# Optimization experiments

Measured on AMD Instinct MI355X. Metric: run time of the kernel, lower is better.

Reference implementation:

```python
import jax, jax.numpy as jnp
import numpy as np

N_USER = 100000
N_ITEM = 100000
N_TAG = 10000
DIM = 128
E_BUYS = 1_000_000
E_REV = 1_000_000
E_TAGS = 1_000_000
W_SCALE = 0.05


def setup_inputs() -> dict:
    key = jax.random.key(0)
    ks = jax.random.split(key, 18)
    inp = {
        "x_user": jax.random.normal(ks[0], (N_USER, DIM), jnp.float32),
        "x_item": jax.random.normal(ks[1], (N_ITEM, DIM), jnp.float32),
        "x_tag": jax.random.normal(ks[2], (N_TAG, DIM), jnp.float32),
        # edge_index per relation: row 0 = src node ids, row 1 = dst node ids
        "ei_buys": jnp.stack([
            jax.random.randint(ks[3], (E_BUYS,), 0, N_USER, jnp.int32),
            jax.random.randint(ks[4], (E_BUYS,), 0, N_ITEM, jnp.int32)]),
        "ei_rev": jnp.stack([
            jax.random.randint(ks[5], (E_REV,), 0, N_ITEM, jnp.int32),
            jax.random.randint(ks[6], (E_REV,), 0, N_USER, jnp.int32)]),
        "ei_tags": jnp.stack([
            jax.random.randint(ks[7], (E_TAGS,), 0, N_TAG, jnp.int32),
            jax.random.randint(ks[8], (E_TAGS,), 0, N_ITEM, jnp.int32)]),
    }
    # SAGEConv params per edge type: lin_l (neighbor agg), lin_r (root), bias
    names = ["buys", "rev", "tags"]
    for i, n in enumerate(names):
        inp[f"Wl_{n}"] = jax.random.normal(ks[9 + 3 * i], (DIM, DIM), jnp.float32) * W_SCALE
        inp[f"Wr_{n}"] = jax.random.normal(ks[10 + 3 * i], (DIM, DIM), jnp.float32) * W_SCALE
        inp[f"b_{n}"] = jnp.zeros((DIM,), jnp.float32)
    return inp


def _sage(x_src, x_dst, ei, Wl, Wr, b):
    """SAGEConv with mean neighbor aggregation: lin_l(mean_j x_j) + lin_r(x_i) + b."""
    n_dst = x_dst.shape[0]
    src, dst = ei[0], ei[1]
    msg_sum = jax.ops.segment_sum(x_src[src], dst, num_segments=n_dst)  # [n_dst, D]
    cnt = jax.ops.segment_sum(jnp.ones(src.shape, x_src.dtype), dst, num_segments=n_dst)
    msg_mean = msg_sum / jnp.maximum(cnt, 1.0)[:, None]
    return msg_mean @ Wl + x_dst @ Wr + b


def reference(x_user, x_item, x_tag, ei_buys, ei_rev, ei_tags,
              Wl_buys, Wr_buys, b_buys,
              Wl_rev, Wr_rev, b_rev,
              Wl_tags, Wr_tags, b_tags):
    # per-relation SAGEConv
    o_item_buys = _sage(x_user, x_item, ei_buys, Wl_buys, Wr_buys, b_buys)
    o_user = _sage(x_item, x_user, ei_rev, Wl_rev, Wr_rev, b_rev)
    o_item_tags = _sage(x_tag, x_item, ei_tags, Wl_tags, Wr_tags, b_tags)
    # HeteroConv aggr='mean' across edge types per destination node type
    out_item = 0.5 * (o_item_buys + o_item_tags)
    out_user = o_user  # single relation into 'user'
    return (out_user, out_item)
```

## Files before the change

### kernel.cpp

```cpp
#include <hip/hip_runtime.h>
#include <hip/hip_bf16.h>
#include <stdint.h>

#define DIM 128
#define NNODE 100000
#define NB 98
#define NBT (3 * NB)
#define T_TILE 8192

typedef __attribute__((ext_vector_type(8))) short short8;
typedef __attribute__((ext_vector_type(4))) float f32x4;

__device__ __forceinline__ unsigned short f32_to_bf16_rne(float f) {
    union { float f; uint32_t u; } v; v.f = f;
    uint32_t u = v.u;
    uint32_t r = u + 0x7FFFu + ((u >> 16) & 1u);
    return (unsigned short)(r >> 16);
}

__global__ void conv_kernel(const float* __restrict__ xu, const float* __restrict__ xi,
                            const float* __restrict__ xt,
                            unsigned short* __restrict__ bu, unsigned short* __restrict__ bi,
                            unsigned short* __restrict__ bt, int nu, int ni, int nt) {
    int idx = blockIdx.x * blockDim.x + threadIdx.x;
    int q_u = nu >> 2, q_i = ni >> 2, q_t = nt >> 2;
    const float* src; unsigned short* dst; int o;
    if (idx < q_u)                { src = xu; dst = bu; o = idx; }
    else if (idx < q_u + q_i)     { src = xi; dst = bi; o = idx - q_u; }
    else if (idx < q_u + q_i+q_t) { src = xt; dst = bt; o = idx - q_u - q_i; }
    else return;
    float4 f = ((const float4*)src)[o];
    ushort4 u;
    u.x = f32_to_bf16_rne(f.x); u.y = f32_to_bf16_rne(f.y);
    u.z = f32_to_bf16_rne(f.z); u.w = f32_to_bf16_rne(f.w);
    ((ushort4*)dst)[o] = u;
}

__global__ __launch_bounds__(256) void coarse_hist(
    const int* __restrict__ ei0, const int* __restrict__ ei1, const int* __restrict__ ei2,
    int E0, int E1, int E2, int* __restrict__ ccnt) {
    __shared__ int h[NBT];
    int Etot = E0 + E1 + E2;
    for (int i = threadIdx.x; i < NBT; i += 256) h[i] = 0;
    __syncthreads();
    for (int e = blockIdx.x * blockDim.x + threadIdx.x; e < Etot; e += gridDim.x * blockDim.x) {
        int rel, le; const int* ei; int E;
        if (e < E0)           { rel = 0; le = e;           ei = ei0; E = E0; }
        else if (e < E0 + E1) { rel = 1; le = e - E0;      ei = ei1; E = E1; }
        else                  { rel = 2; le = e - E0 - E1; ei = ei2; E = E2; }
        int d = ei[E + le];
        atomicAdd(&h[rel * NB + (d >> 10)], 1);
    }
    __syncthreads();
    for (int i = threadIdx.x; i < NBT; i += 256) {
        int c = h[i];
        if (c) atomicAdd(&ccnt[i], c);
    }
}

__global__ __launch_bounds__(512) void coarse_scan(const int* __restrict__ ccnt,
                                                   int* __restrict__ bases,
                                                   int* __restrict__ cursor) {
    __shared__ int s[512];
    int t = threadIdx.x;
    int v = (t < NBT) ? ccnt[t] : 0;
    s[t] = v;
    __syncthreads();
    for (int d = 1; d < 512; d <<= 1) {
        int x = (t >= d) ? s[t - d] : 0;
        __syncthreads();
        s[t] += x;
        __syncthreads();
    }
    int excl = s[t] - v;
    if (t < NBT) { bases[t] = excl; cursor[t] = excl; }
    if (t == NBT) bases[NBT] = excl;
}

__global__ __launch_bounds__(256) void coarse_scatter(
    const int* __restrict__ ei0, const int* __restrict__ ei1, const int* __restrict__ ei2,
    int E0, int E1, int E2, int* __restrict__ cursor, int* __restrict__ pairs) {
    __shared__ int h[NBT], hb[NBT], lc[NBT];
    int Etot = E0 + E1 + E2;
    int ntiles = (Etot + T_TILE - 1) / T_TILE;
    for (int tile = blockIdx.x; tile < ntiles; tile += gridDim.x) {
        int tbase = tile * T_TILE;
        for (int i = threadIdx.x; i < NBT; i += 256) { h[i] = 0; lc[i] = 0; }
        __syncthreads();
        int binreg[32], valreg[32];
        #pragma unroll
        for (int k = 0; k < 32; k++) {
            int e = tbase + k * 256 + threadIdx.x;
            binreg[k] = -1;
            if (e < Etot) {
                int rel, le; const int* ei; int E;
                if (e < E0)           { rel = 0; le = e;           ei = ei0; E = E0; }
                else if (e < E0 + E1) { rel = 1; le = e - E0;      ei = ei1; E = E1; }
                else                  { rel = 2; le = e - E0 - E1; ei = ei2; E = E2; }
                int d = ei[E + le];
                int s = ei[le];
                int bin = rel * NB + (d >> 10);
                binreg[k] = bin;
                valreg[k] = s | ((d & 1023) << 17);
                atomicAdd(&h[bin], 1);
            }
        }
        __syncthreads();
        for (int i = threadIdx.x; i < NBT; i += 256) {
            int c = h[i];
            hb[i] = c ? atomicAdd(&cursor[i], c) : 0;
        }
        __syncthreads();
        #pragma unroll
        for (int k = 0; k < 32; k++) {
            if (binreg[k] >= 0) {
                int bin = binreg[k];
                int pos = hb[bin] + atomicAdd(&lc[bin], 1);
                pairs[pos] = valreg[k];
            }
        }
        __syncthreads();
    }
}

__global__ __launch_bounds__(256) void fine_sort(
    const int* __restrict__ bases, const int* __restrict__ pairs,
    int* __restrict__ off, int* __restrict__ sorted, int N) {
    __shared__ int h[1024], ho[1024], ssum[256];
    int b = blockIdx.x;
    int rel = b / NB, jb = b - rel * NB;
    int ebase = bases[b], ne = bases[b + 1] - ebase;
    int dbase = jb << 10;
    int tid = threadIdx.x;
    for (int i = tid; i < 1024; i += 256) h[i] = 0;
    __syncthreads();
    for (int i = tid; i < ne; i += 256) {
        int dl = pairs[ebase + i] >> 17;
        atomicAdd(&h[dl], 1);
    }
    __syncthreads();
    int v0 = h[tid * 4], v1 = h[tid * 4 + 1], v2 = h[tid * 4 + 2], v3 = h[tid * 4 + 3];
    int tsum = v0 + v1 + v2 + v3;
    ssum[tid] = tsum;
    __syncthreads();
    for (int s = 1; s < 256; s <<= 1) {
        int t = (tid >= s) ? ssum[tid - s] : 0;
        __syncthreads();
        ssum[tid] += t;
        __syncthreads();
    }
    int excl = ssum[tid] - tsum;
    ho[tid * 4] = excl;
    ho[tid * 4 + 1] = excl + v0;
    ho[tid * 4 + 2] = excl + v0 + v1;
    ho[tid * 4 + 3] = excl + v0 + v1 + v2;
    __syncthreads();
    for (int i = tid; i < 1024; i += 256) {
        int d = dbase + i;
        if (d < N) off[rel * N + d] = ebase + ho[i];
        h[i] = 0;
    }
    __syncthreads();
    for (int i = tid; i < ne; i += 256) {
        int p = pairs[ebase + i];
        int dl = p >> 17;
        int pos = ebase + ho[dl] + atomicAdd(&h[dl], 1);
        sorted[pos] = p & 0x1FFFF;
    }
}

__global__ __launch_bounds__(256) void agg_mfma(
    const unsigned short* __restrict__ xb_user, const unsigned short* __restrict__ xb_item,
    const unsigned short* __restrict__ xb_tag,
    const int* __restrict__ sorted, const int* __restrict__ off,
    unsigned short* __restrict__ msg, int N, int Etot) {
    __shared__ __align__(1024) unsigned char smem[4][9216];
    const int wid = threadIdx.x >> 6;
    const int lane = threadIdx.x & 63;
    const int grp = blockIdx.x * 4 + wid;
    const int ngrp = (3 * N) >> 4;
    if (grp >= ngrp) return;
    const int g0 = grp << 4;
    const int rel = (g0 >= 2 * N) ? 2 : ((g0 >= N) ? 1 : 0);
    const unsigned short* xs = (rel == 0) ? xb_user : (rel == 1) ? xb_item : xb_tag;

    unsigned char* stage = smem[wid];
    unsigned char* segb  = smem[wid] + 8192;
    int* bnd = (int*)(smem[wid] + 8192 + 768);

    if (lane < 17) {
        int idx = g0 + lane;
        bnd[lane] = (idx < 3 * N) ? off[idx] : Etot;
    }
    const int b0 = bnd[0];
    const int L  = bnd[16] - b0;
    int nchunk = (L + 31) >> 5;
    if (nchunk > 20) nchunk = 20;
    const int tot = nchunk << 5;

    for (int i = lane; i < tot; i += 64) {
        int k = b0 + i;
        int s = 0;
        #pragma unroll
        for (int t = 1; t <= 16; t++) s += (k >= bnd[t]) ? 1 : 0;
        segb[i] = (unsigned char)s;
    }

    const int jsel = (lane & 7) >> 1;
    const int laneoff = ((lane >> 3) << 5) + ((lane & 1) << 4);
    const unsigned int stage_u =
        (unsigned int)(size_t)(__attribute__((address_space(3))) unsigned char*)stage;
    const unsigned int tb = stage_u + ((lane >> 4) << 11) + ((lane & 15) << 3);
    const unsigned char* xsb = (const unsigned char*)xs;

    f32x4 acc[8];
    #pragma unroll
    for (int i = 0; i < 8; i++) acc[i] = (f32x4){0.f, 0.f, 0.f, 0.f};

    for (int c = 0; c < nchunk; c++) {
        const int cb = b0 + (c << 5);
        int kk = cb + (lane & 31);
        kk = (kk < Etot) ? kk : (Etot - 1);
        const int sv = sorted[kk];
        #pragma unroll
        for (int q = 0; q < 8; q++) {
            int srow = __shfl(sv, (q << 2) + jsel, 64);
            const unsigned char* gp = xsb + (((size_t)srow) << 8) + laneoff;
            __builtin_amdgcn_global_load_lds(
                (const __attribute__((address_space(1))) unsigned int*)gp,
                (__attribute__((address_space(3))) unsigned int*)(stage + (q << 10)),
                16, 0, 0);
        }
        const unsigned long long sg =
            *(const unsigned long long*)(segb + (c << 5) + ((lane >> 4) << 3));
        short8 af;
        #pragma unroll
        for (int j = 0; j < 8; j++)
            af[j] = ((int)((sg >> (j << 3)) & 0xFFull) == (lane & 15)) ? (short)0x3F80 : (short)0;

        asm volatile("s_waitcnt vmcnt(0)" ::: "memory");
        unsigned long long blo[8], bhi[8];
        #pragma unroll
        for (int nt = 0; nt < 8; nt++) {
            asm volatile("ds_read_b64_tr_b16 %0, %2\n\t"
                         "ds_read_b64_tr_b16 %1, %2 offset:1024"
                         : "=&v"(blo[nt]), "=&v"(bhi[nt]) : "v"(tb + (nt << 7)));
        }
        asm volatile("s_waitcnt lgkmcnt(0)" ::: "memory");
        __builtin_amdgcn_sched_barrier(0);
        #pragma unroll
        for (int nt = 0; nt < 8; nt++) {
            union { unsigned long long u[2]; short8 s; } cv;
            cv.u[0] = blo[nt]; cv.u[1] = bhi[nt];
            acc[nt] = __builtin_amdgcn_mfma_f32_16x16x32_bf16(af, cv.s, acc[nt], 0, 0, 0);
        }
    }

    const int gq = lane >> 4;
    const int fc = lane & 15;
    int dg[5];
    #pragma unroll
    for (int r = 0; r < 5; r++) dg[r] = bnd[(gq << 2) + r];
    float invd[4];
    #pragma unroll
    for (int r = 0; r < 4; r++) {
        int d = dg[r + 1] - dg[r];
        invd[r] = 1.0f / (float)(d > 0 ? d : 1);
    }
    unsigned short* outb = (unsigned short*)stage;
    #pragma unroll
    for (int nt = 0; nt < 8; nt++) {
        #pragma unroll
        for (int r = 0; r < 4; r++) {
            outb[(((gq << 2) + r) << 7) + (nt << 4) + fc] =
                f32_to_bf16_rne(acc[nt][r] * invd[r]);
        }
    }
    unsigned char* mp = (unsigned char*)(msg + ((size_t)g0 << 7));
    #pragma unroll
    for (int s = 0; s < 4; s++) {
        uint4 vv = *(const uint4*)(stage + (s << 10) + (lane << 4));
        *(uint4*)(mp + (s << 10) + (lane << 4)) = vv;
    }
}

__global__ void pack_kernel(const float* __restrict__ Wl_b, const float* __restrict__ Wr_b,
                            const float* __restrict__ b_b,
                            const float* __restrict__ Wl_r, const float* __restrict__ Wr_r,
                            const float* __restrict__ b_r,
                            const float* __restrict__ Wl_t, const float* __restrict__ Wr_t,
                            const float* __restrict__ b_t,
                            unsigned short* __restrict__ pw_item,
                            unsigned short* __restrict__ pw_user,
                            float* __restrict__ bias_item, float* __restrict__ bias_user) {
    const int NI = 12 * 8 * 64 * 8;
    const int NU = 8 * 8 * 64 * 8;
    int o = blockIdx.x * blockDim.x + threadIdx.x;
    if (o < NI) {
        int j = o & 7, lane = (o >> 3) & 63, ks = o >> 12;
        int n = ((o >> 9) & 7) * 16 + (lane & 15);
        int k = (ks & 3) * 32 + (lane >> 4) * 8 + j;
        int src = ks >> 2;
        float v;
        if (src == 0)      v = 0.5f * Wl_b[k * DIM + n];
        else if (src == 1) v = 0.5f * Wl_t[k * DIM + n];
        else               v = 0.5f * (Wr_b[k * DIM + n] + Wr_t[k * DIM + n]);
        pw_item[o] = f32_to_bf16_rne(v);
    } else if (o < NI + NU) {
        int oo = o - NI;
        int j = oo & 7, lane = (oo >> 3) & 63, ks = oo >> 12;
        int n = ((oo >> 9) & 7) * 16 + (lane & 15);
        int k = (ks & 3) * 32 + (lane >> 4) * 8 + j;
        float v = ((ks >> 2) == 0) ? Wl_r[k * DIM + n] : Wr_r[k * DIM + n];
        pw_user[oo] = f32_to_bf16_rne(v);
    } else {
        int oo = o - NI - NU;
        if (oo < DIM)            bias_item[oo] = 0.5f * (b_b[oo] + b_t[oo]);
        else if (oo < 2 * DIM)   bias_user[oo - DIM] = b_r[oo - DIM];
    }
}

__global__ __launch_bounds__(256) void gemm_kernel(
    const unsigned short* __restrict__ Abf0,
    const unsigned short* __restrict__ Abf1,
    const unsigned short* __restrict__ Abf2,
    int n_src,
    const unsigned short* __restrict__ packW,
    const float* __restrict__ bias,
    float* __restrict__ out, int M) {
    int wave = threadIdx.x >> 6;
    int lane = threadIdx.x & 63;
    int quad = lane >> 4;
    int l15  = lane & 15;
    int m0   = blockIdx.x * 64 + wave * 16;
    int arow = m0 + l15;
    bool arow_ok = arow < M;
    int nks = n_src * 4;

    f32x4 acc[8];
    #pragma unroll
    for (int i = 0; i < 8; i++) acc[i] = (f32x4){0.f, 0.f, 0.f, 0.f};

    for (int ks = 0; ks < nks; ks++) {
        int src = ks >> 2;
        int kofs = (ks & 3) * 32 + quad * 8;
        short8 afrag;
        const unsigned short* A = (src == 0) ? Abf0 : (src == 1) ? Abf1 : Abf2;
        if (arow_ok) afrag = *(const short8*)(A + (size_t)arow * DIM + kofs);
        else         afrag = (short8){0,0,0,0,0,0,0,0};
        const unsigned short* wp = packW + ((size_t)ks * 8 * 64 + lane) * 8;
        #pragma unroll
        for (int nt = 0; nt < 8; nt++) {
            short8 wfrag = *(const short8*)(wp + (size_t)nt * 64 * 8);
            acc[nt] = __builtin_amdgcn_mfma_f32_16x16x32_bf16(afrag, wfrag, acc[nt], 0, 0, 0);
        }
    }
    #pragma unroll
    for (int nt = 0; nt < 8; nt++) {
        int col = nt * 16 + l15;
        float bv = bias[col];
        #pragma unroll
        for (int r = 0; r < 4; r++) {
            int row = m0 + quad * 4 + r;
            if (row < M) out[(size_t)row * DIM + col] = acc[nt][r] + bv;
        }
    }
}

extern "C" void kernel_launch(void* const* d_in, const int* in_sizes, int n_in,
                              void* d_out, int out_size, void* d_ws, size_t ws_size,
                              hipStream_t stream) {
    const float* x_user = (const float*)d_in[0];
    const float* x_item = (const float*)d_in[1];
    const float* x_tag  = (const float*)d_in[2];
    const int* ei_buys  = (const int*)d_in[3];
    const int* ei_rev   = (const int*)d_in[4];
    const int* ei_tags  = (const int*)d_in[5];
    const float* Wl_b = (const float*)d_in[6];
    const float* Wr_b = (const float*)d_in[7];
    const float* b_b  = (const float*)d_in[8];
    const float* Wl_r = (const float*)d_in[9];
    const float* Wr_r = (const float*)d_in[10];
    const float* b_r  = (const float*)d_in[11];
    const float* Wl_t = (const float*)d_in[12];
    const float* Wr_t = (const float*)d_in[13];
    const float* b_t  = (const float*)d_in[14];

    const int N  = NNODE;
    const int E0 = in_sizes[3] / 2, E1 = in_sizes[4] / 2, E2 = in_sizes[5] / 2;
    const int n_user = in_sizes[0], n_item = in_sizes[1], n_tag = in_sizes[2];

    char* w = (char*)d_ws;
    int* off    = (int*)(w + 1200000);
    int* ccnt   = (int*)(w + 2400000);
    int* bases  = (int*)(w + 2401280);
    int* cursor = (int*)(w + 2402560);
    int* sorted = (int*)(w + 2403840);
    unsigned short* msg = (unsigned short*)(w + 15600000);
    int* pairs  = (int*)(w + 15600000);
    unsigned short* pw_item = (unsigned short*)(w + 92400000);
    unsigned short* pw_user = (unsigned short*)(w + 92498304);
    float* bias_item = (float*)(w + 92563840);
    float* bias_user = (float*)(w + 92564352);
    unsigned short* xb_user = (unsigned short*)(w + 92564992);
    unsigned short* xb_item = (unsigned short*)(w + 118164992);
    unsigned short* xb_tag  = (unsigned short*)(w + 143764992);

    float* out_user = (float*)d_out;
    float* out_item = out_user + (size_t)N * DIM;

    int Etot = E0 + E1 + E2;

    hipMemsetAsync(ccnt, 0, NBT * sizeof(int), stream);

    pack_kernel<<<(49152 + 32768 + 2 * DIM + 255) / 256, 256, 0, stream>>>(
        Wl_b, Wr_b, b_b, Wl_r, Wr_r, b_r, Wl_t, Wr_t, b_t,
        pw_item, pw_user, bias_item, bias_user);

    int tot4 = (n_user + n_item + n_tag) / 4;
    conv_kernel<<<(tot4 + 255) / 256, 256, 0, stream>>>(
        x_user, x_item, x_tag, xb_user, xb_item, xb_tag, n_user, n_item, n_tag);

    coarse_hist<<<512, 256, 0, stream>>>(ei_buys, ei_rev, ei_tags, E0, E1, E2, ccnt);

    coarse_scan<<<1, 512, 0, stream>>>(ccnt, bases, cursor);

    int ntiles = (Etot + T_TILE - 1) / T_TILE;
    coarse_scatter<<<ntiles, 256, 0, stream>>>(
        ei_buys, ei_rev, ei_tags, E0, E1, E2, cursor, pairs);

    fine_sort<<<NBT, 256, 0, stream>>>(bases, pairs, off, sorted, N);

    int ngrp = (3 * N) / 16;
    agg_mfma<<<(ngrp + 3) / 4, 256, 0, stream>>>(
        xb_user, xb_item, xb_tag, sorted, off, msg, N, Etot);

    gemm_kernel<<<(N + 63) / 64, 256, 0, stream>>>(
        msg, msg + 2 * (size_t)N * DIM, xb_item, 3, pw_item, bias_item, out_item, N);

    gemm_kernel<<<(N + 63) / 64, 256, 0, stream>>>(
        msg + (size_t)N * DIM, xb_user, nullptr, 2, pw_user, bias_user, out_user, N);
}
```

Measured before the change: 493.0 us.

## Double-buffer gather-to-LDS in MFMA aggregation with software-pipelined chunk pairs

Restructures the agg_mfma inner loop to process two 32-edge chunks per iteration. Each chunk gets its own 8 KB LDS staging buffer, and the global_load_lds gathers for the next chunk are issued right after the MFMAs on the current buffer, with partial vmcnt waits in place of a full drain. The sorted-index loads are prefetched one iteration ahead. To fit the doubled LDS per wave, the block shrinks from 4 to 3 waves, which changes occupancy. The goal is to hide gather latency behind MFMA work, at the cost of more LDS per wave and extra speculative loads when the chunk count is odd.

```diff
diff --git a/kernel.cpp b/kernel.cpp
--- a/kernel.cpp
+++ b/kernel.cpp
@@ -7,6 +7,8 @@
 #define NB 98
 #define NBT (3 * NB)
 #define T_TILE 8192
+#define AGG_NW 3
+#define AGG_WLDS 17408
 
 typedef __attribute__((ext_vector_type(8))) short short8;
 typedef __attribute__((ext_vector_type(4))) float f32x4;
@@ -169,15 +171,15 @@
     }
 }
 
-__global__ __launch_bounds__(256) void agg_mfma(
+__global__ __launch_bounds__(192) void agg_mfma(
     const unsigned short* __restrict__ xb_user, const unsigned short* __restrict__ xb_item,
     const unsigned short* __restrict__ xb_tag,
     const int* __restrict__ sorted, const int* __restrict__ off,
     unsigned short* __restrict__ msg, int N, int Etot) {
-    __shared__ __align__(1024) unsigned char smem[4][9216];
+    __shared__ __align__(1024) unsigned char smem[AGG_NW][AGG_WLDS];
     const int wid = threadIdx.x >> 6;
     const int lane = threadIdx.x & 63;
-    const int grp = blockIdx.x * 4 + wid;
+    const int grp = blockIdx.x * AGG_NW + wid;
     const int ngrp = (3 * N) >> 4;
     if (grp >= ngrp) return;
     const int g0 = grp << 4;
@@ -185,8 +187,8 @@
     const unsigned short* xs = (rel == 0) ? xb_user : (rel == 1) ? xb_item : xb_tag;
 
     unsigned char* stage = smem[wid];
-    unsigned char* segb  = smem[wid] + 8192;
-    int* bnd = (int*)(smem[wid] + 8192 + 768);
+    unsigned char* segb  = smem[wid] + 16384;
+    int* bnd = (int*)(smem[wid] + 16384 + 640);
 
     if (lane < 17) {
         int idx = g0 + lane;
@@ -196,7 +198,8 @@
     const int L  = bnd[16] - b0;
     int nchunk = (L + 31) >> 5;
     if (nchunk > 20) nchunk = 20;
-    const int tot = nchunk << 5;
+    const int nit = (nchunk + 1) >> 1;
+    const int tot = nit << 6;
 
     for (int i = lane; i < tot; i += 64) {
         int k = b0 + i;
@@ -210,41 +213,51 @@
     const int laneoff = ((lane >> 3) << 5) + ((lane & 1) << 4);
     const unsigned int stage_u =
         (unsigned int)(size_t)(__attribute__((address_space(3))) unsigned char*)stage;
-    const unsigned int tb = stage_u + ((lane >> 4) << 11) + ((lane & 15) << 3);
+    const unsigned int tbA = stage_u + ((lane >> 4) << 11) + ((lane & 15) << 3);
     const unsigned char* xsb = (const unsigned char*)xs;
+    const int clampE = Etot - 1;
+    const int l15 = lane & 15;
+
+    #define ISSUE_G(pvv, half, bufofs) { \
+        _Pragma("unroll") \
+        for (int q = 0; q < 8; q++) { \
+            int srow = __shfl((pvv), ((half) << 5) + (q << 2) + jsel, 64); \
+            const unsigned char* gp = xsb + (((size_t)srow) << 8) + laneoff; \
+            __builtin_amdgcn_global_load_lds( \
+                (const __attribute__((address_space(1))) unsigned int*)gp, \
+                (__attribute__((address_space(3))) unsigned int*)(stage + (bufofs) + (q << 10)), \
+                16, 0, 0); \
+        } }
+
+    #define MK_AF(af, coff) { \
+        const unsigned long long sg = \
+            *(const unsigned long long*)(segb + (coff) + ((lane >> 4) << 3)); \
+        _Pragma("unroll") \
+        for (int j = 0; j < 8; j++) \
+            (af)[j] = ((int)((sg >> (j << 3)) & 0xFFull) == l15) ? (short)0x3F80 : (short)0; }
 
     f32x4 acc[8];
     #pragma unroll
     for (int i = 0; i < 8; i++) acc[i] = (f32x4){0.f, 0.f, 0.f, 0.f};
 
-    for (int c = 0; c < nchunk; c++) {
-        const int cb = b0 + (c << 5);
-        int kk = cb + (lane & 31);
-        kk = (kk < Etot) ? kk : (Etot - 1);
-        const int sv = sorted[kk];
-        #pragma unroll
-        for (int q = 0; q < 8; q++) {
-            int srow = __shfl(sv, (q << 2) + jsel, 64);
-            const unsigned char* gp = xsb + (((size_t)srow) << 8) + laneoff;
-            __builtin_amdgcn_global_load_lds(
-                (const __attribute__((address_space(1))) unsigned int*)gp,
-                (__attribute__((address_space(3))) unsigned int*)(stage + (q << 10)),
-                16, 0, 0);
-        }
-        const unsigned long long sg =
-            *(const unsigned long long*)(segb + (c << 5) + ((lane >> 4) << 3));
-        short8 af;
-        #pragma unroll
-        for (int j = 0; j < 8; j++)
-            af[j] = ((int)((sg >> (j << 3)) & 0xFFull) == (lane & 15)) ? (short)0x3F80 : (short)0;
-
-        asm volatile("s_waitcnt vmcnt(0)" ::: "memory");
+    int pv_use  = sorted[min(b0 + lane, clampE)];
+    int pv_next = sorted[min(b0 + 64 + lane, clampE)];
+    ISSUE_G(pv_use, 0, 0);
+    ISSUE_G(pv_use, 1, 8192);
+
+    for (int i = 0; i < nit; i++) {
+        asm volatile("s_waitcnt vmcnt(16)" ::: "memory");
+        __builtin_amdgcn_sched_barrier(0);
+        int pv = pv_next;
+
+        short8 af0; MK_AF(af0, (i << 6));
+        asm volatile("s_waitcnt vmcnt(8)" ::: "memory");
         unsigned long long blo[8], bhi[8];
         #pragma unroll
         for (int nt = 0; nt < 8; nt++) {
             asm volatile("ds_read_b64_tr_b16 %0, %2\n\t"
                          "ds_read_b64_tr_b16 %1, %2 offset:1024"
-                         : "=&v"(blo[nt]), "=&v"(bhi[nt]) : "v"(tb + (nt << 7)));
+                         : "=&v"(blo[nt]), "=&v"(bhi[nt]) : "v"(tbA + (nt << 7)));
         }
         asm volatile("s_waitcnt lgkmcnt(0)" ::: "memory");
         __builtin_amdgcn_sched_barrier(0);
@@ -252,9 +265,33 @@
         for (int nt = 0; nt < 8; nt++) {
             union { unsigned long long u[2]; short8 s; } cv;
             cv.u[0] = blo[nt]; cv.u[1] = bhi[nt];
-            acc[nt] = __builtin_amdgcn_mfma_f32_16x16x32_bf16(af, cv.s, acc[nt], 0, 0, 0);
-        }
-    }
+            acc[nt] = __builtin_amdgcn_mfma_f32_16x16x32_bf16(af0, cv.s, acc[nt], 0, 0, 0);
+        }
+        pv_next = sorted[min(b0 + ((i + 2) << 6) + lane, clampE)];
+        ISSUE_G(pv, 0, 0);
+
+        short8 af1; MK_AF(af1, (i << 6) + 32);
+        asm volatile("s_waitcnt vmcnt(9)" ::: "memory");
+        #pragma unroll
+        for (int nt = 0; nt < 8; nt++) {
+            asm volatile("ds_read_b64_tr_b16 %0, %2\n\t"
+                         "ds_read_b64_tr_b16 %1, %2 offset:1024"
+                         : "=&v"(blo[nt]), "=&v"(bhi[nt]) : "v"(tbA + 8192 + (nt << 7)));
+        }
+        asm volatile("s_waitcnt lgkmcnt(0)" ::: "memory");
+        __builtin_amdgcn_sched_barrier(0);
+        #pragma unroll
+        for (int nt = 0; nt < 8; nt++) {
+            union { unsigned long long u[2]; short8 s; } cv;
+            cv.u[0] = blo[nt]; cv.u[1] = bhi[nt];
+            acc[nt] = __builtin_amdgcn_mfma_f32_16x16x32_bf16(af1, cv.s, acc[nt], 0, 0, 0);
+        }
+        ISSUE_G(pv, 1, 8192);
+    }
+    asm volatile("s_waitcnt vmcnt(0)" ::: "memory");
+    __builtin_amdgcn_sched_barrier(0);
+    #undef ISSUE_G
+    #undef MK_AF
 
     const int gq = lane >> 4;
     const int fc = lane & 15;
@@ -432,7 +469,7 @@
     fine_sort<<<NBT, 256, 0, stream>>>(bases, pairs, off, sorted, N);
 
     int ngrp = (3 * N) / 16;
-    agg_mfma<<<(ngrp + 3) / 4, 256, 0, stream>>>(
+    agg_mfma<<<(ngrp + AGG_NW - 1) / AGG_NW, 64 * AGG_NW, 0, stream>>>(
         xb_user, xb_item, xb_tag, sorted, off, msg, N, Etot);
 
     gemm_kernel<<<(N + 63) / 64, 256, 0, stream>>>(
```

Measured after the change: 525.9 us. 1.07x slower.

## Fuse neighbor aggregation with output GEMMs into a single kernel

Applied to the files above, without the earlier changes.

Merges the MFMA gather-aggregation kernel and the two weight GEMM kernels into one kernel. Each wave now aggregates its 16 destination rows, writes the mean into XOR-swizzled LDS, and multiplies it by the packed weights right away, adding the root-node term. This removes the bf16 message buffer round trip through global memory and two kernel launches. In exchange, each wave does more work in sequence (item waves run two gathers plus three GEMMs), and the output tail guards are dropped, so N must be a multiple of 16.

```diff
diff --git a/kernel.cpp b/kernel.cpp
--- a/kernel.cpp
+++ b/kernel.cpp
@@ -166,121 +166,6 @@
         int dl = p >> 17;
         int pos = ebase + ho[dl] + atomicAdd(&h[dl], 1);
         sorted[pos] = p & 0x1FFFF;
-    }
-}
-
-__global__ __launch_bounds__(256) void agg_mfma(
-    const unsigned short* __restrict__ xb_user, const unsigned short* __restrict__ xb_item,
-    const unsigned short* __restrict__ xb_tag,
-    const int* __restrict__ sorted, const int* __restrict__ off,
-    unsigned short* __restrict__ msg, int N, int Etot) {
-    __shared__ __align__(1024) unsigned char smem[4][9216];
-    const int wid = threadIdx.x >> 6;
-    const int lane = threadIdx.x & 63;
-    const int grp = blockIdx.x * 4 + wid;
-    const int ngrp = (3 * N) >> 4;
-    if (grp >= ngrp) return;
-    const int g0 = grp << 4;
-    const int rel = (g0 >= 2 * N) ? 2 : ((g0 >= N) ? 1 : 0);
-    const unsigned short* xs = (rel == 0) ? xb_user : (rel == 1) ? xb_item : xb_tag;
-
-    unsigned char* stage = smem[wid];
-    unsigned char* segb  = smem[wid] + 8192;
-    int* bnd = (int*)(smem[wid] + 8192 + 768);
-
-    if (lane < 17) {
-        int idx = g0 + lane;
-        bnd[lane] = (idx < 3 * N) ? off[idx] : Etot;
-    }
-    const int b0 = bnd[0];
-    const int L  = bnd[16] - b0;
-    int nchunk = (L + 31) >> 5;
-    if (nchunk > 20) nchunk = 20;
-    const int tot = nchunk << 5;
-
-    for (int i = lane; i < tot; i += 64) {
-        int k = b0 + i;
-        int s = 0;
-        #pragma unroll
-        for (int t = 1; t <= 16; t++) s += (k >= bnd[t]) ? 1 : 0;
-        segb[i] = (unsigned char)s;
-    }
-
-    const int jsel = (lane & 7) >> 1;
-    const int laneoff = ((lane >> 3) << 5) + ((lane & 1) << 4);
-    const unsigned int stage_u =
-        (unsigned int)(size_t)(__attribute__((address_space(3))) unsigned char*)stage;
-    const unsigned int tb = stage_u + ((lane >> 4) << 11) + ((lane & 15) << 3);
-    const unsigned char* xsb = (const unsigned char*)xs;
-
-    f32x4 acc[8];
-    #pragma unroll
-    for (int i = 0; i < 8; i++) acc[i] = (f32x4){0.f, 0.f, 0.f, 0.f};
-
-    for (int c = 0; c < nchunk; c++) {
-        const int cb = b0 + (c << 5);
-        int kk = cb + (lane & 31);
-        kk = (kk < Etot) ? kk : (Etot - 1);
-        const int sv = sorted[kk];
-        #pragma unroll
-        for (int q = 0; q < 8; q++) {
-            int srow = __shfl(sv, (q << 2) + jsel, 64);
-            const unsigned char* gp = xsb + (((size_t)srow) << 8) + laneoff;
-            __builtin_amdgcn_global_load_lds(
-                (const __attribute__((address_space(1))) unsigned int*)gp,
-                (__attribute__((address_space(3))) unsigned int*)(stage + (q << 10)),
-                16, 0, 0);
-        }
-        const unsigned long long sg =
-            *(const unsigned long long*)(segb + (c << 5) + ((lane >> 4) << 3));
-        short8 af;
-        #pragma unroll
-        for (int j = 0; j < 8; j++)
-            af[j] = ((int)((sg >> (j << 3)) & 0xFFull) == (lane & 15)) ? (short)0x3F80 : (short)0;
-
-        asm volatile("s_waitcnt vmcnt(0)" ::: "memory");
-        unsigned long long blo[8], bhi[8];
-        #pragma unroll
-        for (int nt = 0; nt < 8; nt++) {
-            asm volatile("ds_read_b64_tr_b16 %0, %2\n\t"
-                         "ds_read_b64_tr_b16 %1, %2 offset:1024"
-                         : "=&v"(blo[nt]), "=&v"(bhi[nt]) : "v"(tb + (nt << 7)));
-        }
-        asm volatile("s_waitcnt lgkmcnt(0)" ::: "memory");
-        __builtin_amdgcn_sched_barrier(0);
-        #pragma unroll
-        for (int nt = 0; nt < 8; nt++) {
-            union { unsigned long long u[2]; short8 s; } cv;
-            cv.u[0] = blo[nt]; cv.u[1] = bhi[nt];
-            acc[nt] = __builtin_amdgcn_mfma_f32_16x16x32_bf16(af, cv.s, acc[nt], 0, 0, 0);
-        }
-    }
-
-    const int gq = lane >> 4;
-    const int fc = lane & 15;
-    int dg[5];
-    #pragma unroll
-    for (int r = 0; r < 5; r++) dg[r] = bnd[(gq << 2) + r];
-    float invd[4];
-    #pragma unroll
-    for (int r = 0; r < 4; r++) {
-        int d = dg[r + 1] - dg[r];
-        invd[r] = 1.0f / (float)(d > 0 ? d : 1);
-    }
-    unsigned short* outb = (unsigned short*)stage;
-    #pragma unroll
-    for (int nt = 0; nt < 8; nt++) {
-        #pragma unroll
-        for (int r = 0; r < 4; r++) {
-            outb[(((gq << 2) + r) << 7) + (nt << 4) + fc] =
-                f32_to_bf16_rne(acc[nt][r] * invd[r]);
-        }
-    }
-    unsigned char* mp = (unsigned char*)(msg + ((size_t)g0 << 7));
-    #pragma unroll
-    for (int s = 0; s < 4; s++) {
-        uint4 vv = *(const uint4*)(stage + (s << 10) + (lane << 4));
-        *(uint4*)(mp + (s << 10) + (lane << 4)) = vv;
     }
 }
 
@@ -320,49 +205,170 @@
     }
 }
 
-__global__ __launch_bounds__(256) void gemm_kernel(
-    const unsigned short* __restrict__ Abf0,
-    const unsigned short* __restrict__ Abf1,
-    const unsigned short* __restrict__ Abf2,
-    int n_src,
-    const unsigned short* __restrict__ packW,
-    const float* __restrict__ bias,
-    float* __restrict__ out, int M) {
-    int wave = threadIdx.x >> 6;
-    int lane = threadIdx.x & 63;
-    int quad = lane >> 4;
-    int l15  = lane & 15;
-    int m0   = blockIdx.x * 64 + wave * 16;
-    int arow = m0 + l15;
-    bool arow_ok = arow < M;
-    int nks = n_src * 4;
-
-    f32x4 acc[8];
-    #pragma unroll
-    for (int i = 0; i < 8; i++) acc[i] = (f32x4){0.f, 0.f, 0.f, 0.f};
-
-    for (int ks = 0; ks < nks; ks++) {
-        int src = ks >> 2;
-        int kofs = (ks & 3) * 32 + quad * 8;
-        short8 afrag;
-        const unsigned short* A = (src == 0) ? Abf0 : (src == 1) ? Abf1 : Abf2;
-        if (arow_ok) afrag = *(const short8*)(A + (size_t)arow * DIM + kofs);
-        else         afrag = (short8){0,0,0,0,0,0,0,0};
-        const unsigned short* wp = packW + ((size_t)ks * 8 * 64 + lane) * 8;
+__device__ __forceinline__ void gather_seg(
+    const unsigned short* __restrict__ xs, const int* __restrict__ sorted,
+    const int* bnd, unsigned char* stage, unsigned char* segb,
+    int lane, int Etot, f32x4* acc) {
+    const int b0 = bnd[0];
+    const int L  = bnd[16] - b0;
+    int nchunk = (L + 31) >> 5;
+    if (nchunk > 20) nchunk = 20;
+    const int tot = nchunk << 5;
+    for (int i = lane; i < tot; i += 64) {
+        int k = b0 + i;
+        int s = 0;
+        #pragma unroll
+        for (int t = 1; t <= 16; t++) s += (k >= bnd[t]) ? 1 : 0;
+        segb[i] = (unsigned char)s;
+    }
+    const int jsel = (lane & 7) >> 1;
+    const int laneoff = ((lane >> 3) << 5) + ((lane & 1) << 4);
+    const unsigned int stage_u =
+        (unsigned int)(size_t)(__attribute__((address_space(3))) unsigned char*)stage;
+    const unsigned int tbA = stage_u + ((lane >> 4) << 11) + ((lane & 15) << 3);
+    const unsigned char* xsb = (const unsigned char*)xs;
+    const int l15 = lane & 15;
+    const int kmax = min(max(b0 + L - 1, b0), Etot - 1);
+    for (int c = 0; c < nchunk; c++) {
+        int kk = min(b0 + (c << 5) + (lane & 31), kmax);
+        const int sv = sorted[kk];
+        #pragma unroll
+        for (int q = 0; q < 8; q++) {
+            int srow = __shfl(sv, (q << 2) + jsel, 64);
+            const unsigned char* gp = xsb + (((size_t)srow) << 8) + laneoff;
+            __builtin_amdgcn_global_load_lds(
+                (const __attribute__((address_space(1))) unsigned int*)gp,
+                (__attribute__((address_space(3))) unsigned int*)(stage + (q << 10)),
+                16, 0, 0);
+        }
+        const unsigned long long sg =
+            *(const unsigned long long*)(segb + (c << 5) + ((lane >> 4) << 3));
+        short8 af;
+        #pragma unroll
+        for (int j = 0; j < 8; j++)
+            af[j] = ((int)((sg >> (j << 3)) & 0xFFull) == l15) ? (short)0x3F80 : (short)0;
+        asm volatile("s_waitcnt vmcnt(0)" ::: "memory");
+        unsigned long long blo[8], bhi[8];
+        #pragma unroll
+        for (int nt = 0; nt < 8; nt++) {
+            asm volatile("ds_read_b64_tr_b16 %0, %2\n\t"
+                         "ds_read_b64_tr_b16 %1, %2 offset:1024"
+                         : "=&v"(blo[nt]), "=&v"(bhi[nt]) : "v"(tbA + (nt << 7)));
+        }
+        asm volatile("s_waitcnt lgkmcnt(0)" ::: "memory");
+        __builtin_amdgcn_sched_barrier(0);
+        #pragma unroll
+        for (int nt = 0; nt < 8; nt++) {
+            union { unsigned long long u[2]; short8 s; } cv;
+            cv.u[0] = blo[nt]; cv.u[1] = bhi[nt];
+            acc[nt] = __builtin_amdgcn_mfma_f32_16x16x32_bf16(af, cv.s, acc[nt], 0, 0, 0);
+        }
+    }
+}
+
+__device__ __forceinline__ void pack_wgemm(
+    f32x4* accG, const int* bnd, unsigned char* stage,
+    const unsigned short* __restrict__ packW, int slot0, int lane, f32x4* accO) {
+    const int gq = lane >> 4, fc = lane & 15, l15 = lane & 15, quad = lane >> 4;
+    float invd[4];
+    #pragma unroll
+    for (int r = 0; r < 4; r++) {
+        int d = bnd[(gq << 2) + r + 1] - bnd[(gq << 2) + r];
+        invd[r] = 1.0f / (float)(d > 0 ? d : 1);
+    }
+    #pragma unroll
+    for (int nt = 0; nt < 8; nt++) {
+        #pragma unroll
+        for (int r = 0; r < 4; r++) {
+            int row = (gq << 2) + r;
+            unsigned int b = ((unsigned int)row << 8) + ((unsigned int)((nt << 4) + fc) << 1);
+            b ^= (unsigned int)((row & 15) << 4);
+            *(unsigned short*)(stage + b) = f32_to_bf16_rne(accG[nt][r] * invd[r]);
+        }
+    }
+    #pragma unroll
+    for (int ksl = 0; ksl < 4; ksl++) {
+        unsigned int rb = ((unsigned int)l15 << 8) + (ksl << 6) + (quad << 4);
+        rb ^= (unsigned int)(l15 << 4);
+        short8 afrag = *(const short8*)(stage + rb);
+        const unsigned short* wp = packW + ((size_t)(slot0 + ksl) * 8 * 64 + lane) * 8;
         #pragma unroll
         for (int nt = 0; nt < 8; nt++) {
             short8 wfrag = *(const short8*)(wp + (size_t)nt * 64 * 8);
-            acc[nt] = __builtin_amdgcn_mfma_f32_16x16x32_bf16(afrag, wfrag, acc[nt], 0, 0, 0);
-        }
+            accO[nt] = __builtin_amdgcn_mfma_f32_16x16x32_bf16(afrag, wfrag, accO[nt], 0, 0, 0);
+        }
+    }
+}
+
+__device__ __forceinline__ void root_wgemm(
+    const unsigned short* __restrict__ xroot, int g0,
+    const unsigned short* __restrict__ packW, int slot0, int lane, f32x4* accO) {
+    const int l15 = lane & 15, quad = lane >> 4;
+    #pragma unroll
+    for (int ksl = 0; ksl < 4; ksl++) {
+        short8 afrag = *(const short8*)(xroot + (size_t)(g0 + l15) * DIM + (ksl * 32 + quad * 8));
+        const unsigned short* wp = packW + ((size_t)(slot0 + ksl) * 8 * 64 + lane) * 8;
+        #pragma unroll
+        for (int nt = 0; nt < 8; nt++) {
+            short8 wfrag = *(const short8*)(wp + (size_t)nt * 64 * 8);
+            accO[nt] = __builtin_amdgcn_mfma_f32_16x16x32_bf16(afrag, wfrag, accO[nt], 0, 0, 0);
+        }
+    }
+}
+
+__global__ __launch_bounds__(256) void fused_agg(
+    const unsigned short* __restrict__ xb_user, const unsigned short* __restrict__ xb_item,
+    const unsigned short* __restrict__ xb_tag,
+    const int* __restrict__ sorted, const int* __restrict__ off,
+    const unsigned short* __restrict__ pw_item, const unsigned short* __restrict__ pw_user,
+    const float* __restrict__ bias_item, const float* __restrict__ bias_user,
+    float* __restrict__ out, int N, int Etot) {
+    __shared__ __align__(1024) unsigned char smem[4][9216];
+    const int wid = threadIdx.x >> 6;
+    const int lane = threadIdx.x & 63;
+    const int grp = blockIdx.x * 4 + wid;
+    const int Gi = N >> 4;
+    if (grp >= 2 * Gi) return;
+    unsigned char* stage = smem[wid];
+    unsigned char* segb  = smem[wid] + 8192;
+    int* bnd = (int*)(smem[wid] + 8192 + 640);
+    const int quad = lane >> 4, l15 = lane & 15;
+
+    f32x4 accO[8], accG[8];
+    #pragma unroll
+    for (int i = 0; i < 8; i++) accO[i] = (f32x4){0.f, 0.f, 0.f, 0.f};
+
+    float* op; const float* bias; int g0;
+    if (grp < Gi) {
+        g0 = grp << 4;
+        if (lane < 17) bnd[lane] = off[g0 + lane];
+        #pragma unroll
+        for (int i = 0; i < 8; i++) accG[i] = (f32x4){0.f, 0.f, 0.f, 0.f};
+        gather_seg(xb_user, sorted, bnd, stage, segb, lane, Etot, accG);
+        pack_wgemm(accG, bnd, stage, pw_item, 0, lane, accO);
+        if (lane < 17) { int idx = 2 * N + g0 + lane; bnd[lane] = (idx < 3 * N) ? off[idx] : Etot; }
+        #pragma unroll
+        for (int i = 0; i < 8; i++) accG[i] = (f32x4){0.f, 0.f, 0.f, 0.f};
+        gather_seg(xb_tag, sorted, bnd, stage, segb, lane, Etot, accG);
+        pack_wgemm(accG, bnd, stage, pw_item, 4, lane, accO);
+        root_wgemm(xb_item, g0, pw_item, 8, lane, accO);
+        op = out + (size_t)N * DIM; bias = bias_item;
+    } else {
+        g0 = (grp - Gi) << 4;
+        if (lane < 17) bnd[lane] = off[N + g0 + lane];
+        #pragma unroll
+        for (int i = 0; i < 8; i++) accG[i] = (f32x4){0.f, 0.f, 0.f, 0.f};
+        gather_seg(xb_item, sorted, bnd, stage, segb, lane, Etot, accG);
+        pack_wgemm(accG, bnd, stage, pw_user, 0, lane, accO);
+        root_wgemm(xb_user, g0, pw_user, 4, lane, accO);
+        op = out; bias = bias_user;
     }
     #pragma unroll
     for (int nt = 0; nt < 8; nt++) {
-        int col = nt * 16 + l15;
-        float bv = bias[col];
+        float bv = bias[nt * 16 + l15];
         #pragma unroll
         for (int r = 0; r < 4; r++) {
-            int row = m0 + quad * 4 + r;
-            if (row < M) out[(size_t)row * DIM + col] = acc[nt][r] + bv;
+            op[(size_t)(g0 + quad * 4 + r) * DIM + nt * 16 + l15] = accO[nt][r] + bv;
         }
     }
 }
@@ -396,7 +402,6 @@
     int* bases  = (int*)(w + 2401280);
     int* cursor = (int*)(w + 2402560);
     int* sorted = (int*)(w + 2403840);
-    unsigned short* msg = (unsigned short*)(w + 15600000);
     int* pairs  = (int*)(w + 15600000);
     unsigned short* pw_item = (unsigned short*)(w + 92400000);
     unsigned short* pw_user = (unsigned short*)(w + 92498304);
@@ -406,8 +411,7 @@
     unsigned short* xb_item = (unsigned short*)(w + 118164992);
     unsigned short* xb_tag  = (unsigned short*)(w + 143764992);
 
-    float* out_user = (float*)d_out;
-    float* out_item = out_user + (size_t)N * DIM;
+    float* out_all = (float*)d_out;
 
     int Etot = E0 + E1 + E2;
 
@@ -431,13 +435,8 @@
 
     fine_sort<<<NBT, 256, 0, stream>>>(bases, pairs, off, sorted, N);
 
-    int ngrp = (3 * N) / 16;
-    agg_mfma<<<(ngrp + 3) / 4, 256, 0, stream>>>(
-        xb_user, xb_item, xb_tag, sorted, off, msg, N, Etot);
-
-    gemm_kernel<<<(N + 63) / 64, 256, 0, stream>>>(
-        msg, msg + 2 * (size_t)N * DIM, xb_item, 3, pw_item, bias_item, out_item, N);
-
-    gemm_kernel<<<(N + 63) / 64, 256, 0, stream>>>(
-        msg + (size_t)N * DIM, xb_user, nullptr, 2, pw_user, bias_user, out_user, N);
-}
+    int ngrp = 2 * (N / 16);
+    fused_agg<<<(ngrp + 3) / 4, 256, 0, stream>>>(
+        xb_user, xb_item, xb_tag, sorted, off, pw_item, pw_user,
+        bias_item, bias_user, out_all, N, Etot);
+}
```

After: 465.5 us. -5.6%, faster.
